# Performance work log

Hardware: AMD Instinct MI355X
Metric: run time of the kernel (lower is better)

Reference implementation:

```python
import jax, jax.numpy as jnp
import numpy as np

B, T, V = 64, 4096, 64
NGLIMPSE = 32
GRAN_SCALES = (1, 5)  # hard-coded in getGlimpseTimesteps
NGRAN = len(GRAN_SCALES)
NHID = 2048
GWIDTH = 0.1


def setup_inputs() -> dict:
    key = jax.random.key(0)
    k1, k2, k3, k4, k5 = jax.random.split(key, 5)
    # times sorted ascending per sample (scipy interp1d assumption)
    time = jnp.sort(jax.random.uniform(k1, (B, T)) * 100.0, axis=1)
    vals = jax.random.normal(k2, (B, T, V))
    masks = (jax.random.uniform(k3, (B, T, V)) < 0.5).astype(jnp.int32)
    lengths = jnp.full((B,), T, dtype=jnp.int32)
    l_t = jax.random.uniform(k4, (B, 1), minval=0.1, maxval=0.9)
    fan_in = V * NGRAN * NGLIMPSE + 1
    W = jax.random.normal(k5, (NHID, fan_in)) / np.sqrt(fan_in)
    b = jnp.zeros((NHID,), jnp.float32)
    return {"vals": vals, "time": time, "masks": masks,
            "lengths": lengths, "l_t": l_t, "W": W, "b": b}


def _interp_one(t, v, m, r):
    """Masked 1D linear interp of (t[m], v[m]) at queries r.
    Constant fill (first/last valid value) outside bounds; 0 if no valid point."""
    ts = jnp.where(m, t, jnp.inf)
    order = jnp.argsort(ts)          # stable: valid (already sorted) times first
    tsort = ts[order]                # [T], inf tail for invalid entries
    vsort = v[order]
    n = m.sum()
    idx = jnp.searchsorted(tsort, r, side='right')
    i1 = jnp.clip(idx, 1, jnp.maximum(n - 1, 1))
    i0 = i1 - 1
    t0, t1 = tsort[i0], tsort[i1]
    v0, v1 = vsort[i0], vsort[i1]
    w = jnp.clip((r - t0) / jnp.where(t1 > t0, t1 - t0, 1.0), 0.0, 1.0)
    y = v0 + w * (v1 - v0)
    last = jnp.maximum(n - 1, 0)
    y = jnp.where(r <= tsort[0], vsort[0],
                  jnp.where(r >= tsort[last], vsort[last], y))
    return jnp.where(n == 0, 0.0, y)


def _glimpses(vals, time, masks, l_t):
    # [NGRAN, NGLIMPSE] offsets: linspace(-gwidth*i/2, gwidth*i/2, nglimpse)
    lin = jnp.stack([jnp.linspace(-GWIDTH * i / 2.0, GWIDTH * i / 2.0, NGLIMPSE)
                     for i in GRAN_SCALES])

    def per_sample(t, v, m, l):
        # denormalize by per-sample max time; granularity-major flatten
        r = ((lin + l) * t.max()).reshape(-1)          # [NGRAN*NGLIMPSE]
        return jax.vmap(lambda vv, mm: _interp_one(t, vv, mm, r),
                        in_axes=(1, 1))(v, m)          # [V, NGRAN*NGLIMPSE]

    return jax.vmap(per_sample)(time, vals, masks.astype(bool), l_t[:, 0])


def reference(vals, time, masks, lengths, l_t, W, b):
    g = _glimpses(vals, time, masks, l_t).reshape(vals.shape[0], -1)  # [B, V*NGRAN*NGLIMPSE]
    grep = jnp.concatenate([g, l_t], axis=1) @ W.T + b                # [B, NHID]
    return grep, g[:, g.shape[1] // 2]
```

## Files before the change

kernel.cpp:

```cpp
#include <hip/hip_runtime.h>
#include <hip/hip_bf16.h>

#define B    64
#define T    4096
#define V    64
#define NQ   64
#define NHID 2048
#define KDIM 4096
#define FAN  4097

#define NT     16
#define SPLITS 8

typedef __attribute__((ext_vector_type(8))) short bf16x8;
typedef __attribute__((ext_vector_type(4))) float f32x4;

static __device__ __forceinline__ short f2bf(float x) {
    union { float f; unsigned u; } c; c.f = x;
    unsigned r = c.u + 0x7fff + ((c.u >> 16) & 1);
    return (short)(r >> 16);
}

__global__ __launch_bounds__(64) void glimpse_kernel(
    const float* __restrict__ vals, const float* __restrict__ time_,
    const int* __restrict__ masks, const float* __restrict__ l_t,
    unsigned short* __restrict__ g_bf, float* __restrict__ out2,
    float* __restrict__ out)
{
    const int b = blockIdx.x;
    const int q = blockIdx.y;
    const int v = threadIdx.x;

    if (v < 32) out[(size_t)b * NHID + q * 32 + v] = 0.0f;

    const float* t = time_ + (size_t)b * T;
    const float tmax = t[T - 1];

    const int   j = q & 31;
    const float s = (q < 32) ? 1.0f : 5.0f;
    const float a = 0.5f * 0.1f * s;
    const float step = (2.0f * a) / 31.0f;
    float lin = (j == 31) ? a : (-a + step * (float)j);
    const float r = (lin + l_t[b]) * tmax;

    int lo = 0, hi = T;
    while (lo < hi) {
        int mid = (lo + hi) >> 1;
        if (t[mid] > r) hi = mid; else lo = mid + 1;
    }
    const int p = lo;

    const int*   m  = masks + (size_t)b * T * V + v;
    const float* vv = vals  + (size_t)b * T * V + v;

    int i0 = -1;
    for (int i = p - 1; i >= 0; --i) {
        if (m[(size_t)i * V] != 0) { i0 = i; break; }
    }
    int i1 = -1;
    for (int i = p; i < T; ++i) {
        if (m[(size_t)i * V] != 0) { i1 = i; break; }
    }

    float y;
    if (i0 < 0 && i1 < 0) {
        y = 0.0f;
    } else if (i0 < 0) {
        y = vv[(size_t)i1 * V];
    } else if (i1 < 0) {
        y = vv[(size_t)i0 * V];
    } else {
        float t0 = t[i0], t1 = t[i1];
        float v0 = vv[(size_t)i0 * V], v1 = vv[(size_t)i1 * V];
        float den = (t1 > t0) ? (t1 - t0) : 1.0f;
        float w = (r - t0) / den;
        w = fminf(fmaxf(w, 0.0f), 1.0f);
        y = v0 + w * (v1 - v0);
    }

    const int k = v * NQ + q;
    g_bf[(size_t)b * KDIM + k] = (unsigned short)f2bf(y);
    if (k == KDIM / 2) out2[b] = y;
}

__global__ __launch_bounds__(256) void gemm_mfma(
    const unsigned short* __restrict__ g_bf, const float* __restrict__ l_t,
    const float* __restrict__ W, const float* __restrict__ bias,
    float* __restrict__ out)
{
    __shared__ float part[4][B][NT];
    const int lane = threadIdx.x & 63;
    const int wave = threadIdx.x >> 6;
    const int l15  = lane & 15;
    const int lk   = lane >> 4;
    const int hbase = blockIdx.x * NT;
    const int kbase = blockIdx.y * (KDIM / SPLITS) + wave * (KDIM / SPLITS / 4);

    const float* wrow = W + (size_t)(hbase + l15) * FAN;

    f32x4 acc[4];
    #pragma unroll
    for (int mt = 0; mt < 4; ++mt) acc[mt] = (f32x4){0.f, 0.f, 0.f, 0.f};

    #pragma unroll
    for (int ks = 0; ks < KDIM / SPLITS / 4; ks += 32) {
        const int k = kbase + ks + lk * 8;

        bf16x8 bfrag;
        #pragma unroll
        for (int e = 0; e < 8; ++e) bfrag[e] = f2bf(wrow[k + e]);

        #pragma unroll
        for (int mt = 0; mt < 4; ++mt) {
            const bf16x8 afrag =
                *(const bf16x8*)(g_bf + (size_t)(mt * 16 + l15) * KDIM + k);
            acc[mt] = __builtin_amdgcn_mfma_f32_16x16x32_bf16(afrag, bfrag, acc[mt], 0, 0, 0);
        }
    }

    #pragma unroll
    for (int mt = 0; mt < 4; ++mt) {
        #pragma unroll
        for (int rreg = 0; rreg < 4; ++rreg) {
            const int b = mt * 16 + lk * 4 + rreg;
            part[wave][b][l15] = acc[mt][rreg];
        }
    }
    __syncthreads();

    for (int o = threadIdx.x; o < B * NT; o += 256) {
        const int b = o >> 4, hoff = o & 15;
        const int h = hbase + hoff;
        float v = part[0][b][hoff] + part[1][b][hoff]
                + part[2][b][hoff] + part[3][b][hoff];
        if (blockIdx.y == 0)
            v += bias[h] + l_t[b] * W[(size_t)h * FAN + KDIM];
        atomicAdd(&out[(size_t)b * NHID + h], v);
    }
}

extern "C" void kernel_launch(void* const* d_in, const int* in_sizes, int n_in,
                              void* d_out, int out_size, void* d_ws, size_t ws_size,
                              hipStream_t stream) {
    const float* vals  = (const float*)d_in[0];
    const float* time_ = (const float*)d_in[1];
    const int*   masks = (const int*)d_in[2];
    const float* l_t   = (const float*)d_in[4];
    const float* W     = (const float*)d_in[5];
    const float* bias  = (const float*)d_in[6];

    float* out  = (float*)d_out;
    float* out2 = out + (size_t)B * NHID;
    unsigned short* g_bf = (unsigned short*)d_ws;

    dim3 g1(B, NQ);
    glimpse_kernel<<<g1, 64, 0, stream>>>(vals, time_, masks, l_t, g_bf, out2, out);

    dim3 g2(NHID / NT, SPLITS);
    gemm_mfma<<<g2, 256, 0, stream>>>(g_bf, l_t, W, bias, out);
}
```

Measured before the change: 35.68 us.

## Stage time row in LDS, batch glimpses per block, window-scan masks

The glimpse kernel now handles 8 query points per 512-thread block and first copies the sample's whole time row into shared memory, so the binary search and the t0/t1 reads hit LDS instead of global memory. The sequential mask scan is replaced by an unrolled 32-entry window load around the search position, using clz/ctz to find the neighbouring valid indices and falling back to a linear scan only when the window has none. Results are staged in a small LDS tile and written as 16-byte vectors, which coalesces the bf16 stores. The costs are a 16 KB LDS load per block and 32 mask loads per thread even when the nearest valid entries are adjacent.

```diff
diff --git a/kernel.cpp b/kernel.cpp
--- a/kernel.cpp
+++ b/kernel.cpp
@@ -11,6 +11,7 @@
 
 #define NT     16
 #define SPLITS 8
+#define QPB    8
 
 typedef __attribute__((ext_vector_type(8))) short bf16x8;
 typedef __attribute__((ext_vector_type(4))) float f32x4;
@@ -21,20 +22,33 @@
     return (short)(r >> 16);
 }
 
-__global__ __launch_bounds__(64) void glimpse_kernel(
+__global__ __launch_bounds__(512) void glimpse_kernel(
     const float* __restrict__ vals, const float* __restrict__ time_,
     const int* __restrict__ masks, const float* __restrict__ l_t,
     unsigned short* __restrict__ g_bf, float* __restrict__ out2,
     float* __restrict__ out)
 {
-    const int b = blockIdx.x;
-    const int q = blockIdx.y;
-    const int v = threadIdx.x;
+    __shared__ float tlds[T];
+    __shared__ unsigned short gtile[V][QPB];
+    const int b   = blockIdx.x;
+    const int qb  = blockIdx.y;
+    const int tid = threadIdx.x;
+    const int v   = tid & 63;
+    const int w   = tid >> 6;
+    const int q   = qb * QPB + w;
 
-    if (v < 32) out[(size_t)b * NHID + q * 32 + v] = 0.0f;
+    if (tid < NHID / QPB) out[(size_t)b * NHID + qb * (NHID / QPB) + tid] = 0.0f;
 
-    const float* t = time_ + (size_t)b * T;
-    const float tmax = t[T - 1];
+    {
+        const float4* t4  = (const float4*)(time_ + (size_t)b * T);
+        float4* tl4 = (float4*)tlds;
+        #pragma unroll
+        for (int i = 0; i < T / 4 / 512; ++i)
+            tl4[tid + i * 512] = t4[tid + i * 512];
+    }
+    __syncthreads();
+
+    const float tmax = tlds[T - 1];
 
     const int   j = q & 31;
     const float s = (q < 32) ? 1.0f : 5.0f;
@@ -46,41 +60,65 @@
     int lo = 0, hi = T;
     while (lo < hi) {
         int mid = (lo + hi) >> 1;
-        if (t[mid] > r) hi = mid; else lo = mid + 1;
+        if (tlds[mid] > r) hi = mid; else lo = mid + 1;
     }
     const int p = lo;
 
-    const int*   m  = masks + (size_t)b * T * V + v;
-    const float* vv = vals  + (size_t)b * T * V + v;
+    const int* mrow = masks + (size_t)b * T * V + v;
 
-    int i0 = -1;
-    for (int i = p - 1; i >= 0; --i) {
-        if (m[(size_t)i * V] != 0) { i0 = i; break; }
-    }
-    int i1 = -1;
-    for (int i = p; i < T; ++i) {
-        if (m[(size_t)i * V] != 0) { i1 = i; break; }
+    const int lorow = p - 16;
+    unsigned wm = 0;
+    #pragma unroll
+    for (int jj = 0; jj < 32; ++jj) {
+        const int i = lorow + jj;
+        int mv = 0;
+        if (i >= 0 && i < T) mv = mrow[(size_t)i * V];
+        wm |= (mv != 0 ? 1u : 0u) << jj;
     }
 
+    const unsigned lo16 = wm & 0xffffu;
+    const unsigned hi16 = wm >> 16;
+    int i0, i1;
+    if (lo16) {
+        i0 = lorow + (31 - __builtin_clz(lo16));
+    } else {
+        i0 = -1;
+        for (int i = lorow - 1; i >= 0; --i)
+            if (mrow[(size_t)i * V] != 0) { i0 = i; break; }
+    }
+    if (hi16) {
+        i1 = p + __builtin_ctz(hi16);
+    } else {
+        i1 = -1;
+        for (int i = p + 16; i < T; ++i)
+            if (mrow[(size_t)i * V] != 0) { i1 = i; break; }
+    }
+
+    const float* vrow = vals + (size_t)b * T * V + v;
     float y;
     if (i0 < 0 && i1 < 0) {
         y = 0.0f;
     } else if (i0 < 0) {
-        y = vv[(size_t)i1 * V];
+        y = vrow[(size_t)i1 * V];
     } else if (i1 < 0) {
-        y = vv[(size_t)i0 * V];
+        y = vrow[(size_t)i0 * V];
     } else {
-        float t0 = t[i0], t1 = t[i1];
-        float v0 = vv[(size_t)i0 * V], v1 = vv[(size_t)i1 * V];
+        float t0 = tlds[i0], t1 = tlds[i1];
+        float v0 = vrow[(size_t)i0 * V], v1 = vrow[(size_t)i1 * V];
         float den = (t1 > t0) ? (t1 - t0) : 1.0f;
-        float w = (r - t0) / den;
-        w = fminf(fmaxf(w, 0.0f), 1.0f);
-        y = v0 + w * (v1 - v0);
+        float ww = (r - t0) / den;
+        ww = fminf(fmaxf(ww, 0.0f), 1.0f);
+        y = v0 + ww * (v1 - v0);
     }
 
-    const int k = v * NQ + q;
-    g_bf[(size_t)b * KDIM + k] = (unsigned short)f2bf(y);
-    if (k == KDIM / 2) out2[b] = y;
+    gtile[v][w] = (unsigned short)f2bf(y);
+    if (v * NQ + q == KDIM / 2) out2[b] = y;
+    __syncthreads();
+
+    if (tid < V) {
+        *(bf16x8*)(g_bf + (size_t)b * KDIM + tid * NQ + qb * QPB) =
+            *(const bf16x8*)&gtile[tid][0];
+    }
 }
 
 __global__ __launch_bounds__(256) void gemm_mfma(
@@ -153,8 +191,8 @@
     float* out2 = out + (size_t)B * NHID;
     unsigned short* g_bf = (unsigned short*)d_ws;
 
-    dim3 g1(B, NQ);
-    glimpse_kernel<<<g1, 64, 0, stream>>>(vals, time_, masks, l_t, g_bf, out2, out);
+    dim3 g1(B, NQ / QPB);
+    glimpse_kernel<<<g1, 512, 0, stream>>>(vals, time_, masks, l_t, g_bf, out2, out);
 
     dim3 g2(NHID / NT, SPLITS);
     gemm_mfma<<<g2, 256, 0, stream>>>(g_bf, l_t, W, bias, out);
```

New measurement: 37.17 us. 4.2% more time.

## Stage A and W tiles in LDS with coalesced loads and retile GEMM

Applied to the files above, without the earlier changes.

The GEMM kernel now loads the activation tile and a converted bf16 W tile into shared memory with coalesced accesses, then each wave computes a 16-row slice against 32 output columns from LDS. Tile sizes change to NT=32 and SPLITS=16, and the in-block cross-wave reduction is replaced by direct atomic adds per wave. The aim is to replace the strided per-lane W reads, which stepped across rows of length 4097, with coalesced row reads, and to reuse the A tile through LDS. The trade-off is more atomics on the output, since there are more K splits, and the cost of staging through LDS.

```diff
diff --git a/kernel.cpp b/kernel.cpp
--- a/kernel.cpp
+++ b/kernel.cpp
@@ -9,8 +9,10 @@
 #define KDIM 4096
 #define FAN  4097
 
-#define NT     16
-#define SPLITS 8
+#define NT     32
+#define SPLITS 16
+#define KC     (KDIM / SPLITS)
+#define LDA    (KC + 8)
 
 typedef __attribute__((ext_vector_type(8))) short bf16x8;
 typedef __attribute__((ext_vector_type(4))) float f32x4;
@@ -88,54 +90,61 @@
     const float* __restrict__ W, const float* __restrict__ bias,
     float* __restrict__ out)
 {
-    __shared__ float part[4][B][NT];
-    const int lane = threadIdx.x & 63;
-    const int wave = threadIdx.x >> 6;
+    __shared__ unsigned short alds[B][LDA];
+    __shared__ unsigned short wlds[NT][LDA];
+    const int tid  = threadIdx.x;
+    const int lane = tid & 63;
+    const int wave = tid >> 6;
     const int l15  = lane & 15;
     const int lk   = lane >> 4;
     const int hbase = blockIdx.x * NT;
-    const int kbase = blockIdx.y * (KDIM / SPLITS) + wave * (KDIM / SPLITS / 4);
-
-    const float* wrow = W + (size_t)(hbase + l15) * FAN;
-
-    f32x4 acc[4];
-    #pragma unroll
-    for (int mt = 0; mt < 4; ++mt) acc[mt] = (f32x4){0.f, 0.f, 0.f, 0.f};
+    const int s     = blockIdx.y;
+    const int kbase = s * KC;
 
     #pragma unroll
-    for (int ks = 0; ks < KDIM / SPLITS / 4; ks += 32) {
-        const int k = kbase + ks + lk * 8;
+    for (int i = 0; i < (B * KC) / (256 * 8); ++i) {
+        const int c   = tid + i * 256;
+        const int row = c >> 5;
+        const int c8  = (c & 31) << 3;
+        *(bf16x8*)&alds[row][c8] =
+            *(const bf16x8*)(g_bf + (size_t)row * KDIM + kbase + c8);
+    }
+    #pragma unroll
+    for (int i = 0; i < (NT * KC) / 256; ++i) {
+        const int c   = tid + i * 256;
+        const int row = c >> 8;
+        const int col = c & (KC - 1);
+        wlds[row][col] =
+            (unsigned short)f2bf(W[(size_t)(hbase + row) * FAN + kbase + col]);
+    }
+    __syncthreads();
 
-        bf16x8 bfrag;
+    f32x4 acc[2];
+    acc[0] = (f32x4){0.f, 0.f, 0.f, 0.f};
+    acc[1] = (f32x4){0.f, 0.f, 0.f, 0.f};
+
+    #pragma unroll
+    for (int ks = 0; ks < KC; ks += 32) {
+        const int kl = ks + lk * 8;
+        const bf16x8 afrag = *(const bf16x8*)&alds[wave * 16 + l15][kl];
         #pragma unroll
-        for (int e = 0; e < 8; ++e) bfrag[e] = f2bf(wrow[k + e]);
-
-        #pragma unroll
-        for (int mt = 0; mt < 4; ++mt) {
-            const bf16x8 afrag =
-                *(const bf16x8*)(g_bf + (size_t)(mt * 16 + l15) * KDIM + k);
-            acc[mt] = __builtin_amdgcn_mfma_f32_16x16x32_bf16(afrag, bfrag, acc[mt], 0, 0, 0);
+        for (int nt = 0; nt < 2; ++nt) {
+            const bf16x8 bfrag = *(const bf16x8*)&wlds[nt * 16 + l15][kl];
+            acc[nt] = __builtin_amdgcn_mfma_f32_16x16x32_bf16(afrag, bfrag, acc[nt], 0, 0, 0);
         }
     }
 
     #pragma unroll
-    for (int mt = 0; mt < 4; ++mt) {
+    for (int nt = 0; nt < 2; ++nt) {
+        const int h = hbase + nt * 16 + l15;
         #pragma unroll
-        for (int rreg = 0; rreg < 4; ++rreg) {
-            const int b = mt * 16 + lk * 4 + rreg;
-            part[wave][b][l15] = acc[mt][rreg];
+        for (int r = 0; r < 4; ++r) {
+            const int b = wave * 16 + lk * 4 + r;
+            float v = acc[nt][r];
+            if (s == 0)
+                v += bias[h] + l_t[b] * W[(size_t)h * FAN + KDIM];
+            atomicAdd(&out[(size_t)b * NHID + h], v);
         }
-    }
-    __syncthreads();
-
-    for (int o = threadIdx.x; o < B * NT; o += 256) {
-        const int b = o >> 4, hoff = o & 15;
-        const int h = hbase + hoff;
-        float v = part[0][b][hoff] + part[1][b][hoff]
-                + part[2][b][hoff] + part[3][b][hoff];
-        if (blockIdx.y == 0)
-            v += bias[h] + l_t[b] * W[(size_t)h * FAN + KDIM];
-        atomicAdd(&out[(size_t)b * NHID + h], v);
     }
 }
 
```

Measured after the change: 31.16 us. 1.15x faster.

## Stage GEMM operands in swizzled LDS via direct global-to-LDS loads

Applied to the files above, without the earlier changes.

The GEMM kernel now copies each block's activation and weight K-chunk into LDS using direct global-to-LDS 16-byte loads, with an XOR swizzle to avoid bank conflicts. Weights are converted to bf16 with packed convert instructions instead of per-element scalar rounding. Each wave now owns one 16-row batch tile, and the K split doubles to 16. The aim is to replace strided, poorly coalesced per-lane weight reads with coalesced bulk transfers. The cost is twice as many atomic additions into the output. The 16-byte weight loads are also not 16-byte aligned, because the row stride of 4097 floats is odd.

```diff
diff --git a/kernel.cpp b/kernel.cpp
--- a/kernel.cpp
+++ b/kernel.cpp
@@ -10,7 +10,8 @@
 #define FAN  4097
 
 #define NT     16
-#define SPLITS 8
+#define SPLITS 16
+#define KC     256
 
 typedef __attribute__((ext_vector_type(8))) short bf16x8;
 typedef __attribute__((ext_vector_type(4))) float f32x4;
@@ -19,6 +20,18 @@
     union { float f; unsigned u; } c; c.f = x;
     unsigned r = c.u + 0x7fff + ((c.u >> 16) & 1);
     return (short)(r >> 16);
+}
+
+static __device__ __forceinline__ void load_lds16(const void* g, void* l) {
+    __builtin_amdgcn_global_load_lds(
+        (const __attribute__((address_space(1))) void*)g,
+        (__attribute__((address_space(3))) void*)l, 16, 0, 0);
+}
+
+static __device__ __forceinline__ unsigned cvt_pk(float lo, float hi) {
+    unsigned r;
+    asm volatile("v_cvt_pk_bf16_f32 %0, %1, %2" : "=v"(r) : "v"(lo), "v"(hi));
+    return r;
 }
 
 __global__ __launch_bounds__(64) void glimpse_kernel(
@@ -88,52 +101,63 @@
     const float* __restrict__ W, const float* __restrict__ bias,
     float* __restrict__ out)
 {
-    __shared__ float part[4][B][NT];
-    const int lane = threadIdx.x & 63;
-    const int wave = threadIdx.x >> 6;
-    const int l15  = lane & 15;
-    const int lk   = lane >> 4;
+    __shared__ unsigned short alds[B * KC];
+    __shared__ float wlds[NT * KC];
+    const int tid  = threadIdx.x;
+    const int l    = tid & 63;
+    const int w    = tid >> 6;
+    const int l15  = l & 15;
+    const int lk   = l >> 4;
     const int hbase = blockIdx.x * NT;
-    const int kbase = blockIdx.y * (KDIM / SPLITS) + wave * (KDIM / SPLITS / 4);
-
-    const float* wrow = W + (size_t)(hbase + l15) * FAN;
-
-    f32x4 acc[4];
-    #pragma unroll
-    for (int mt = 0; mt < 4; ++mt) acc[mt] = (f32x4){0.f, 0.f, 0.f, 0.f};
+    const int s     = blockIdx.y;
+    const int kbase = s * KC;
 
     #pragma unroll
-    for (int ks = 0; ks < KDIM / SPLITS / 4; ks += 32) {
-        const int k = kbase + ks + lk * 8;
+    for (int i = 0; i < 8; ++i) {
+        const int m = w * 8 + i;
+        const int r = 2 * m + (l >> 5);
+        const int c = (l & 31) ^ (r & 7);
+        load_lds16(g_bf + (size_t)r * KDIM + kbase + c * 8,
+                   alds + m * 512);
+    }
+    #pragma unroll
+    for (int i = 0; i < 4; ++i) {
+        const int r = w * 4 + i;
+        const int c = l ^ (r & 7);
+        load_lds16(W + (size_t)(hbase + r) * FAN + kbase + c * 4,
+                   wlds + r * KC);
+    }
+    asm volatile("s_waitcnt vmcnt(0)" ::: "memory");
+    __syncthreads();
 
-        bf16x8 bfrag;
-        #pragma unroll
-        for (int e = 0; e < 8; ++e) bfrag[e] = f2bf(wrow[k + e]);
+    f32x4 acc = (f32x4){0.f, 0.f, 0.f, 0.f};
+    const int ra = w * 16 + l15;
+    const int rb = l15;
 
-        #pragma unroll
-        for (int mt = 0; mt < 4; ++mt) {
-            const bf16x8 afrag =
-                *(const bf16x8*)(g_bf + (size_t)(mt * 16 + l15) * KDIM + k);
-            acc[mt] = __builtin_amdgcn_mfma_f32_16x16x32_bf16(afrag, bfrag, acc[mt], 0, 0, 0);
-        }
+    #pragma unroll
+    for (int ks = 0; ks < 8; ++ks) {
+        const int ca = ks * 4 + lk;
+        const bf16x8 afrag =
+            *(const bf16x8*)(alds + ra * KC + ((ca ^ (ra & 7)) << 3));
+
+        const int cb = ks * 8 + lk * 2;
+        const float4 f0 = *(const float4*)(wlds + rb * KC + (((cb    ) ^ (rb & 7)) << 2));
+        const float4 f1 = *(const float4*)(wlds + rb * KC + (((cb + 1) ^ (rb & 7)) << 2));
+        union { unsigned u[4]; bf16x8 v; } bb;
+        bb.u[0] = cvt_pk(f0.x, f0.y);
+        bb.u[1] = cvt_pk(f0.z, f0.w);
+        bb.u[2] = cvt_pk(f1.x, f1.y);
+        bb.u[3] = cvt_pk(f1.z, f1.w);
+
+        acc = __builtin_amdgcn_mfma_f32_16x16x32_bf16(afrag, bb.v, acc, 0, 0, 0);
     }
 
+    const int h = hbase + l15;
     #pragma unroll
-    for (int mt = 0; mt < 4; ++mt) {
-        #pragma unroll
-        for (int rreg = 0; rreg < 4; ++rreg) {
-            const int b = mt * 16 + lk * 4 + rreg;
-            part[wave][b][l15] = acc[mt][rreg];
-        }
-    }
-    __syncthreads();
-
-    for (int o = threadIdx.x; o < B * NT; o += 256) {
-        const int b = o >> 4, hoff = o & 15;
-        const int h = hbase + hoff;
-        float v = part[0][b][hoff] + part[1][b][hoff]
-                + part[2][b][hoff] + part[3][b][hoff];
-        if (blockIdx.y == 0)
+    for (int rr = 0; rr < 4; ++rr) {
+        const int b = w * 16 + lk * 4 + rr;
+        float v = acc[rr];
+        if (s == 0)
             v += bias[h] + l_t[b] * W[(size_t)h * FAN + KDIM];
         atomicAdd(&out[(size_t)b * NHID + h], v);
     }
```

Measured after the change: 30.04 us. 15.8% less time.
